# Optimization experiments

Hardware: AMD Instinct MI355X
Metric: run time of the kernel (lower is better)

Reference implementation:

```python
import jax, jax.numpy as jnp
import numpy as np
from jax.ops import segment_sum, segment_max

N_NODES = 50000
N_EDGES = 640000
N_GRAPHS = 128
IN_DIM = 128
HID = 128
OUT_DIM = 2


def setup_inputs() -> dict:
    key = jax.random.key(0)
    ks = jax.random.split(key, 16)
    x = jax.random.normal(ks[0], (N_NODES, IN_DIM), dtype=jnp.float32)
    edge_index = jax.random.randint(ks[1], (2, N_EDGES), 0, N_NODES, dtype=jnp.int64)
    batch = jnp.sort(jax.random.randint(ks[2], (N_NODES,), 0, N_GRAPHS, dtype=jnp.int64))
    s = 0.05
    return {
        "x": x,
        "edge_index": edge_index,
        "batch": batch,
        "w0": jax.random.normal(ks[3], (HID, IN_DIM), dtype=jnp.float32) * s,
        "b0": jnp.zeros((HID,), jnp.float32),
        "w1": jax.random.normal(ks[4], (HID, HID), dtype=jnp.float32) * s,
        "b1": jnp.zeros((HID,), jnp.float32),
        "w2": jax.random.normal(ks[5], (HID, HID), dtype=jnp.float32) * s,
        "b2": jnp.zeros((HID,), jnp.float32),
        "gate_w": jax.random.normal(ks[6], (1, HID), dtype=jnp.float32) * s,
        "gate_b": jnp.zeros((1,), jnp.float32),
        "lin_w": jax.random.normal(ks[7], (2 * HID, HID), dtype=jnp.float32) * s,
        "lin_b": jnp.zeros((2 * HID,), jnp.float32),
        "cls_w": jax.random.normal(ks[8], (OUT_DIM, 2 * HID), dtype=jnp.float32) * s,
        "cls_b": jnp.zeros((OUT_DIM,), jnp.float32),
    }


def _gcn_norm(edge_index, n):
    # add self loops, symmetric normalization D^-1/2 (A+I) D^-1/2
    loop = jnp.arange(n, dtype=edge_index.dtype)
    row = jnp.concatenate([edge_index[0], loop])
    col = jnp.concatenate([edge_index[1], loop])
    deg = segment_sum(jnp.ones_like(col, dtype=jnp.float32), col, num_segments=n)
    dis = jnp.where(deg > 0, jax.lax.rsqrt(deg), 0.0)
    norm = dis[row] * dis[col]
    return row, col, norm


def _gcn_conv(x, w, b, row, col, norm, n):
    xw = x @ w.T + b                     # [N, hid]
    msg = norm[:, None] * xw[row]        # gather + scale, [E+N, hid]
    return segment_sum(msg, col, num_segments=n)


def _att_pool(x, gate_w, gate_b, batch, g):
    gate = x @ gate_w.T + gate_b         # [N, 1]
    m = segment_max(gate, batch, num_segments=g)        # [G, 1]
    e = jnp.exp(gate - m[batch])
    s = segment_sum(e, batch, num_segments=g)           # [G, 1]
    alpha = e / s[batch]                                # [N, 1]
    return segment_sum(alpha * x, batch, num_segments=g)  # [G, hid]


def reference(x, edge_index, batch, w0, b0, w1, b1, w2, b2,
              gate_w, gate_b, lin_w, lin_b, cls_w, cls_b):
    n = N_NODES
    g = N_GRAPHS
    row, col, norm = _gcn_norm(edge_index, n)
    hg = None
    for w, b in ((w0, b0), (w1, b1), (w2, b2)):
        x = _gcn_conv(x, w, b, row, col, norm, n)
        x = jax.nn.relu(x)  # dropout is identity in eval mode
        pooled = _att_pool(x, gate_w, gate_b, batch, g)
        hg = pooled if hg is None else hg + pooled
    out = jax.nn.relu(hg @ lin_w.T + lin_b)
    return out @ cls_w.T + cls_b
```

## Files before the change

### kernel.cpp

```cpp
#include <hip/hip_runtime.h>
#include <hip/hip_bf16.h>
#include <float.h>

#define N_NODES  50000
#define N_EDGES  640000
#define N_GRAPHS 128
#define DIM      128
#define CAP      64
#define ZROW     N_NODES
#define NSLICE   8
#define SLICE_W  6250
#define NCHUNK   256
#define CHUNK_E  2500
#define GEMM_BLKS 512
#define POOL_BLKS 1024
#define AGG_BLKS  (8*782)

typedef __attribute__((ext_vector_type(8))) short bf16x8;
typedef __attribute__((ext_vector_type(4))) float f32x4;

__device__ __forceinline__ unsigned short f2bf(float f){
  unsigned int u = __float_as_uint(f);
  u += 0x7fffu + ((u >> 16) & 1u);
  return (unsigned short)(u >> 16);
}
__device__ __forceinline__ float2 up2(unsigned int p){
  return make_float2(__uint_as_float(p << 16),
                     __uint_as_float(p & 0xffff0000u));
}

__global__ __launch_bounds__(256) void zero_misc(int* __restrict__ cnt,
    unsigned int* __restrict__ z0, unsigned int* __restrict__ z1){
  int i = blockIdx.x*256 + threadIdx.x;
  if (i < N_NODES) cnt[i] = 0;
  else if (i < N_NODES + 64) z0[i - N_NODES] = 0;
  else if (i < N_NODES + 128) z1[i - N_NODES - 64] = 0;
}

__global__ __launch_bounds__(256) void scatter_sliced(
    const int* __restrict__ ei, int* __restrict__ cnt, int* __restrict__ srcb){
  int slice = blockIdx.x & (NSLICE-1);
  int chunk = blockIdx.x >> 3;
  int e0 = chunk * CHUNK_E;
  for (int e = e0 + threadIdx.x; e < e0 + CHUNK_E; e += 256){
    int c = ei[N_EDGES + e];
    if (c / SLICE_W == slice){
      int r = ei[e];
      int pos = atomicAdd(&cnt[c], 1);
      srcb[(c << 6) + pos] = r;
    }
  }
}

__global__ __launch_bounds__(256) void prep(
    const int* __restrict__ cnt, float* __restrict__ dis,
    const int* __restrict__ batch, int* __restrict__ gs,
    const float* __restrict__ w0, const float* __restrict__ w1,
    const float* __restrict__ w2, unsigned int* __restrict__ o0,
    unsigned int* __restrict__ o1, unsigned int* __restrict__ o2){
  int b = blockIdx.x, tid = threadIdx.x;
  if (b < 196){
    int i = b*256 + tid;
    if (i < N_NODES){
      dis[i] = 1.0f / sqrtf((float)(cnt[i] + 1));
      int bb = batch[i];
      int bp = (i == 0) ? -1 : batch[i-1];
      for (int g = bp + 1; g <= bb; ++g) gs[g] = i;
      if (i == N_NODES - 1)
        for (int g = bb + 1; g <= N_GRAPHS; ++g) gs[g] = N_NODES;
    }
  } else {
    int i = (b - 196)*256 + tid;
    if (i < 3*8192){
      int a = i >> 13, j = i & 8191;
      const float* src = (a == 0) ? w0 : (a == 1) ? w1 : w2;
      unsigned int* dst = (a == 0) ? o0 : (a == 1) ? o1 : o2;
      float2 v = ((const float2*)src)[j];
      dst[j] = (unsigned int)f2bf(v.x) | ((unsigned int)f2bf(v.y) << 16);
    }
  }
}

__device__ __forceinline__ void gemm_body_bf(int wid,
    const unsigned short* __restrict__ A, const unsigned short* __restrict__ Wb,
    const float* __restrict__ bias, const float* __restrict__ dis,
    unsigned short* __restrict__ C, int total_waves){
  int lane = threadIdx.x & 63;
  int l15 = lane & 15, l4 = lane >> 4;
  bf16x8 wf[8][4];
  #pragma unroll
  for (int ob = 0; ob < 8; ++ob)
    #pragma unroll
    for (int ks = 0; ks < 4; ++ks)
      wf[ob][ks] = *(const bf16x8*)&Wb[(ob*16 + l15)*128 + ks*32 + l4*8];
  float bv[8];
  #pragma unroll
  for (int ob = 0; ob < 8; ++ob) bv[ob] = bias[ob*16 + l15];
  for (int t = wid; t < N_NODES/16; t += total_waves){
    int row0 = t*16;
    bf16x8 af[4];
    #pragma unroll
    for (int ks = 0; ks < 4; ++ks)
      af[ks] = *(const bf16x8*)&A[(size_t)(row0 + l15)*128 + ks*32 + l4*8];
    f32x4 acc[8];
    #pragma unroll
    for (int ob = 0; ob < 8; ++ob) acc[ob] = (f32x4){0.f,0.f,0.f,0.f};
    #pragma unroll
    for (int ks = 0; ks < 4; ++ks)
      #pragma unroll
      for (int ob = 0; ob < 8; ++ob)
        acc[ob] = __builtin_amdgcn_mfma_f32_16x16x32_bf16(af[ks], wf[ob][ks],
                                                          acc[ob], 0, 0, 0);
    float dv[4];
    #pragma unroll
    for (int r = 0; r < 4; ++r) dv[r] = dis[row0 + l4*4 + r];
    #pragma unroll
    for (int ob = 0; ob < 8; ++ob)
      #pragma unroll
      for (int r = 0; r < 4; ++r)
        C[(size_t)(row0 + l4*4 + r)*128 + ob*16 + l15] =
            f2bf((acc[ob][r] + bv[ob]) * dv[r]);
  }
}

__global__ __launch_bounds__(256, 2) void gemm_f32(
    const float* __restrict__ A, const unsigned short* __restrict__ Wb,
    const float* __restrict__ bias, const float* __restrict__ dis,
    unsigned short* __restrict__ C, int total_waves){
  int lane = threadIdx.x & 63;
  int wid = blockIdx.x*4 + (threadIdx.x >> 6);
  int l15 = lane & 15, l4 = lane >> 4;
  bf16x8 wf[8][4];
  #pragma unroll
  for (int ob = 0; ob < 8; ++ob)
    #pragma unroll
    for (int ks = 0; ks < 4; ++ks)
      wf[ob][ks] = *(const bf16x8*)&Wb[(ob*16 + l15)*128 + ks*32 + l4*8];
  float bv[8];
  #pragma unroll
  for (int ob = 0; ob < 8; ++ob) bv[ob] = bias[ob*16 + l15];
  for (int t = wid; t < N_NODES/16; t += total_waves){
    int row0 = t*16;
    bf16x8 af[4];
    #pragma unroll
    for (int ks = 0; ks < 4; ++ks){
      const float4* ap = (const float4*)&A[(size_t)(row0 + l15)*128 + ks*32 + l4*8];
      float4 fa = ap[0], fb = ap[1];
      bf16x8 v;
      v[0]=(short)f2bf(fa.x); v[1]=(short)f2bf(fa.y);
      v[2]=(short)f2bf(fa.z); v[3]=(short)f2bf(fa.w);
      v[4]=(short)f2bf(fb.x); v[5]=(short)f2bf(fb.y);
      v[6]=(short)f2bf(fb.z); v[7]=(short)f2bf(fb.w);
      af[ks] = v;
    }
    f32x4 acc[8];
    #pragma unroll
    for (int ob = 0; ob < 8; ++ob) acc[ob] = (f32x4){0.f,0.f,0.f,0.f};
    #pragma unroll
    for (int ks = 0; ks < 4; ++ks)
      #pragma unroll
      for (int ob = 0; ob < 8; ++ob)
        acc[ob] = __builtin_amdgcn_mfma_f32_16x16x32_bf16(af[ks], wf[ob][ks],
                                                          acc[ob], 0, 0, 0);
    float dv[4];
    #pragma unroll
    for (int r = 0; r < 4; ++r) dv[r] = dis[row0 + l4*4 + r];
    #pragma unroll
    for (int ob = 0; ob < 8; ++ob)
      #pragma unroll
      for (int r = 0; r < 4; ++r)
        C[(size_t)(row0 + l4*4 + r)*128 + ob*16 + l15] =
            f2bf((acc[ob][r] + bv[ob]) * dv[r]);
  }
}

__device__ __forceinline__ void pool_body(int pbid,
    const unsigned int* __restrict__ x, const float* __restrict__ gate,
    const int* __restrict__ gs, float* __restrict__ hgp,
    float* __restrict__ ssum){
  int g = pbid >> 3, q = pbid & 7, tid = threadIdx.x;
  int s = gs[g], e = gs[g+1];
  __shared__ float red[256];
  __shared__ float2 red2[4][64];
  float m = -FLT_MAX;
  for (int i = s + tid; i < e; i += 256) m = fmaxf(m, gate[i]);
  red[tid] = m; __syncthreads();
  for (int st = 128; st > 0; st >>= 1){
    if (tid < st) red[tid] = fmaxf(red[tid], red[tid+st]);
    __syncthreads();
  }
  m = red[0]; __syncthreads();
  float p = 0.f;
  for (int i = s + tid; i < e; i += 256) p += __expf(gate[i] - m);
  red[tid] = p; __syncthreads();
  for (int st = 128; st > 0; st >>= 1){
    if (tid < st) red[tid] += red[tid+st];
    __syncthreads();
  }
  if (tid == 0 && q == 0) ssum[g] = red[0];
  int d2 = tid & 63, rg = tid >> 6;
  float ax = 0.f, ay = 0.f;
  for (int i = s + q*4 + rg; i < e; i += 32){
    float a = __expf(gate[i] - m);
    float2 u = up2(x[(size_t)i*64 + d2]);
    ax += a*u.x; ay += a*u.y;
  }
  red2[rg][d2] = make_float2(ax, ay);
  __syncthreads();
  if (tid < 64){
    float2 r0 = red2[0][tid], r1 = red2[1][tid],
           r2 = red2[2][tid], r3 = red2[3][tid];
    hgp[(size_t)pbid*128 + 2*tid    ] = r0.x + r1.x + r2.x + r3.x;
    hgp[(size_t)pbid*128 + 2*tid + 1] = r0.y + r1.y + r2.y + r3.y;
  }
}

__global__ __launch_bounds__(256, 2) void pool_gemm(
    const unsigned int* __restrict__ xb, const float* __restrict__ gate,
    const int* __restrict__ gs, float* __restrict__ hgp,
    float* __restrict__ ssum,
    const unsigned short* __restrict__ Wb, const float* __restrict__ bias,
    const float* __restrict__ dis, unsigned short* __restrict__ xwout){
  if (blockIdx.x < GEMM_BLKS){
    int wid = blockIdx.x*4 + (threadIdx.x >> 6);
    gemm_body_bf(wid, (const unsigned short*)xb, Wb, bias, dis, xwout,
                 GEMM_BLKS*4);
  } else {
    pool_body(blockIdx.x - GEMM_BLKS, xb, gate, gs, hgp, ssum);
  }
}

__global__ __launch_bounds__(256) void att_pool(
    const unsigned int* __restrict__ xb, const float* __restrict__ gate,
    const int* __restrict__ gs, float* __restrict__ hgp,
    float* __restrict__ ssum){
  pool_body(blockIdx.x, xb, gate, gs, hgp, ssum);
}

__global__ __launch_bounds__(256) void aggregate_bf(
    const uint4* __restrict__ xw4,
    const int* __restrict__ cnt, const int* __restrict__ srcb,
    const float* __restrict__ dis,
    uint4* __restrict__ xout4, const float* __restrict__ gw,
    const float* __restrict__ gb, float* __restrict__ gate){
  int tid  = threadIdx.x;
  int lane = tid & 63;
  int wv   = tid >> 6;
  int quad = wv >> 1;
  int par  = wv & 1;
  int sub  = lane >> 4, l16 = lane & 15;
  int slice = blockIdx.x & 7, within = blockIdx.x >> 3;
  int loc   = within*8 + quad*4 + sub;
  bool valid = loc < SLICE_W;
  int node  = slice*SLICE_W + (valid ? loc : SLICE_W-1);
  int n     = valid ? cnt[node] : 0;
  int base  = node << 6;
  float acc[8];
  #pragma unroll
  for (int i = 0; i < 8; ++i) acc[i] = 0.f;
  if (par == 0 && valid){
    uint4 v = xw4[node*16 + l16];
    float2 a0 = up2(v.x), a1 = up2(v.y), a2 = up2(v.z), a3 = up2(v.w);
    acc[0]=a0.x; acc[1]=a0.y; acc[2]=a1.x; acc[3]=a1.y;
    acc[4]=a2.x; acc[5]=a2.y; acc[6]=a3.x; acc[7]=a3.y;
  }
  for (int e = par*8; e < n; e += 16){
    int4 sa = *(const int4*)&srcb[base + e];
    int4 sb = *(const int4*)&srcb[base + e + 4];
    int r0 = (e   < n) ? sa.x : ZROW;
    int r1 = (e+1 < n) ? sa.y : ZROW;
    int r2 = (e+2 < n) ? sa.z : ZROW;
    int r3 = (e+3 < n) ? sa.w : ZROW;
    int r4 = (e+4 < n) ? sb.x : ZROW;
    int r5 = (e+5 < n) ? sb.y : ZROW;
    int r6 = (e+6 < n) ? sb.z : ZROW;
    int r7 = (e+7 < n) ? sb.w : ZROW;
    uint4 u0 = xw4[r0*16 + l16];
    uint4 u1 = xw4[r1*16 + l16];
    uint4 u2 = xw4[r2*16 + l16];
    uint4 u3 = xw4[r3*16 + l16];
    uint4 u4 = xw4[r4*16 + l16];
    uint4 u5 = xw4[r5*16 + l16];
    uint4 u6 = xw4[r6*16 + l16];
    uint4 u7 = xw4[r7*16 + l16];
    #define ACC8(U) { \
      float2 b0=up2(U.x), b1=up2(U.y), b2=up2(U.z), b3=up2(U.w); \
      acc[0]+=b0.x; acc[1]+=b0.y; acc[2]+=b1.x; acc[3]+=b1.y;    \
      acc[4]+=b2.x; acc[5]+=b2.y; acc[6]+=b3.x; acc[7]+=b3.y; }
    ACC8(u0) ACC8(u1) ACC8(u2) ACC8(u3)
    ACC8(u4) ACC8(u5) ACC8(u6) ACC8(u7)
    #undef ACC8
  }
  __shared__ float comb[2][64][9];
  if (par == 1){
    #pragma unroll
    for (int i = 0; i < 8; ++i) comb[quad][lane][i] = acc[i];
  }
  __syncthreads();
  if (par == 0 && valid){
    float d = dis[node];
    #pragma unroll
    for (int i = 0; i < 8; ++i)
      acc[i] = fmaxf(d*(acc[i] + comb[quad][lane][i]), 0.f);
    uint4 o;
    o.x = (unsigned int)f2bf(acc[0]) | ((unsigned int)f2bf(acc[1]) << 16);
    o.y = (unsigned int)f2bf(acc[2]) | ((unsigned int)f2bf(acc[3]) << 16);
    o.z = (unsigned int)f2bf(acc[4]) | ((unsigned int)f2bf(acc[5]) << 16);
    o.w = (unsigned int)f2bf(acc[6]) | ((unsigned int)f2bf(acc[7]) << 16);
    xout4[node*16 + l16] = o;
    const float4* gw4 = (const float4*)gw;
    float4 g0 = gw4[l16*2], g1 = gw4[l16*2 + 1];
    float p = acc[0]*g0.x + acc[1]*g0.y + acc[2]*g0.z + acc[3]*g0.w
            + acc[4]*g1.x + acc[5]*g1.y + acc[6]*g1.z + acc[7]*g1.w;
    p += __shfl_xor(p, 1, 64);
    p += __shfl_xor(p, 2, 64);
    p += __shfl_xor(p, 4, 64);
    p += __shfl_xor(p, 8, 64);
    if (l16 == 0) gate[node] = p + gb[0];
  }
}

__global__ __launch_bounds__(256) void head(const float* __restrict__ hgp,
    const float* __restrict__ ssum,
    const float* __restrict__ lw, const float* __restrict__ lb,
    const float* __restrict__ cw, const float* __restrict__ cb,
    float* __restrict__ out){
  int g = blockIdx.x, tid = threadIdx.x;
  __shared__ float h[128];
  __shared__ float t1[256];
  __shared__ float red[256];
  if (tid < 128){
    float hv = 0.f;
    #pragma unroll
    for (int L = 0; L < 3; ++L){
      const float* hb = hgp + (size_t)(L*POOL_BLKS + 8*g)*128;
      float pp = 0.f;
      #pragma unroll
      for (int q = 0; q < 8; ++q) pp += hb[q*128 + tid];
      float sv = ssum[L*N_GRAPHS + g];
      hv += (sv > 0.f) ? pp/sv : 0.f;
    }
    h[tid] = hv;
  }
  __syncthreads();
  const float* wr = lw + tid*128;
  float a = 0.f;
  for (int k = 0; k < 128; ++k) a += h[k]*wr[k];
  a = fmaxf(a + lb[tid], 0.f);
  t1[tid] = a;
  __syncthreads();
  int o = tid >> 7, j = tid & 127;
  float p = t1[j]*cw[o*256 + j] + t1[j+128]*cw[o*256 + j + 128];
  red[tid] = p; __syncthreads();
  for (int st = 64; st > 0; st >>= 1){
    if (j < st) red[tid] += red[tid+st];
    __syncthreads();
  }
  if (j == 0) out[g*2 + o] = red[tid] + cb[o];
}

extern "C" void kernel_launch(void* const* d_in, const int* in_sizes, int n_in,
                              void* d_out, int out_size, void* d_ws, size_t ws_size,
                              hipStream_t stream){
  const float* x   = (const float*)d_in[0];
  const int*   ei  = (const int*)d_in[1];
  const int* batch = (const int*)d_in[2];
  const float* w0  = (const float*)d_in[3];
  const float* b0  = (const float*)d_in[4];
  const float* w1  = (const float*)d_in[5];
  const float* b1  = (const float*)d_in[6];
  const float* w2  = (const float*)d_in[7];
  const float* b2  = (const float*)d_in[8];
  const float* gw  = (const float*)d_in[9];
  const float* gb  = (const float*)d_in[10];
  const float* lw  = (const float*)d_in[11];
  const float* lb  = (const float*)d_in[12];
  const float* cw  = (const float*)d_in[13];
  const float* cb  = (const float*)d_in[14];
  float* out = (float*)d_out;
  (void)in_sizes; (void)n_in; (void)out_size; (void)ws_size;

  char* ws = (char*)d_ws;
  size_t off = 0;
  auto alloc = [&](size_t bytes)->char*{
    char* p = ws + off;
    off = (off + bytes + 255) & ~(size_t)255;
    return p;
  };
  float* dis    = (float*)alloc((size_t)N_NODES*4);
  unsigned int* xw   = (unsigned int*)alloc((size_t)(N_NODES+1)*64*4);
  unsigned int* xbuf = (unsigned int*)alloc((size_t)(N_NODES+1)*64*4);
  unsigned int* Wb0  = (unsigned int*)alloc((size_t)DIM*64*4);
  unsigned int* Wb1  = (unsigned int*)alloc((size_t)DIM*64*4);
  unsigned int* Wb2  = (unsigned int*)alloc((size_t)DIM*64*4);
  float* gate  = (float*)alloc((size_t)N_NODES*4);
  float* hgp   = (float*)alloc((size_t)3*POOL_BLKS*DIM*4);
  float* ssum  = (float*)alloc((size_t)3*N_GRAPHS*4);
  int*   gs    = (int*)alloc((size_t)(N_GRAPHS+1)*4);
  int*   cnt   = (int*)alloc((size_t)N_NODES*4);
  int*   srcb  = (int*)alloc(((size_t)N_NODES*CAP + 64)*4);

  const int T = 256;
  zero_misc     <<<(N_NODES+128+T-1)/T, T, 0, stream>>>(cnt,
                    xw + (size_t)ZROW*64, xbuf + (size_t)ZROW*64);
  scatter_sliced<<<NCHUNK*NSLICE, T, 0, stream>>>(ei, cnt, srcb);
  prep          <<<196 + 96, T, 0, stream>>>(cnt, dis, batch, gs,
                                             w0, w1, w2, Wb0, Wb1, Wb2);

  gemm_f32<<<GEMM_BLKS, 256, 0, stream>>>(x, (const unsigned short*)Wb0, b0,
                                          dis, (unsigned short*)xw, GEMM_BLKS*4);
  aggregate_bf<<<AGG_BLKS, 256, 0, stream>>>((const uint4*)xw, cnt, srcb, dis,
                                             (uint4*)xbuf, gw, gb, gate);
  pool_gemm<<<GEMM_BLKS + POOL_BLKS, 256, 0, stream>>>(
      xbuf, gate, gs, hgp, ssum,
      (const unsigned short*)Wb1, b1, dis, (unsigned short*)xw);
  aggregate_bf<<<AGG_BLKS, 256, 0, stream>>>((const uint4*)xw, cnt, srcb, dis,
                                             (uint4*)xbuf, gw, gb, gate);
  pool_gemm<<<GEMM_BLKS + POOL_BLKS, 256, 0, stream>>>(
      xbuf, gate, gs, hgp + (size_t)POOL_BLKS*DIM, ssum + N_GRAPHS,
      (const unsigned short*)Wb2, b2, dis, (unsigned short*)xw);
  aggregate_bf<<<AGG_BLKS, 256, 0, stream>>>((const uint4*)xw, cnt, srcb, dis,
                                             (uint4*)xbuf, gw, gb, gate);
  att_pool<<<POOL_BLKS, 256, 0, stream>>>(xbuf, gate, gs,
                                          hgp + (size_t)2*POOL_BLKS*DIM,
                                          ssum + 2*N_GRAPHS);
  head<<<N_GRAPHS, 256, 0, stream>>>(hgp, ssum, lw, lb, cw, cb, out);
}
```

Baseline: 198.7 us.

## Split node feature matrices into four 32-column planes for cache-local gather aggregation

Node feature buffers are stored as four planes of 32 bf16 columns each, so each aggregation block gathers only one 64-byte quarter-row per neighbor. Blocks are assigned per plane, which shrinks the working set per plane and should improve L2 hit rates for the random edge gathers. Each node uses 4 lanes per plane, replacing the two-wave split and LDS combine. The gate dot product is now stored as four partial sums that the pooling step adds together. This brings more blocks, repeated neighbor-list reads across planes, and extra gate reads in pooling.

```diff
diff --git a/kernel.cpp b/kernel.cpp
--- a/kernel.cpp
+++ b/kernel.cpp
@@ -8,13 +8,15 @@
 #define DIM      128
 #define CAP      64
 #define ZROW     N_NODES
+#define NROWS    (N_NODES+1)
 #define NSLICE   8
 #define SLICE_W  6250
 #define NCHUNK   256
 #define CHUNK_E  2500
 #define GEMM_BLKS 512
 #define POOL_BLKS 1024
-#define AGG_BLKS  (8*782)
+#define AGG_CHUNKS 782
+#define AGG_BLKS  (8*391)
 
 typedef __attribute__((ext_vector_type(8))) short bf16x8;
 typedef __attribute__((ext_vector_type(4))) float f32x4;
@@ -33,8 +35,13 @@
     unsigned int* __restrict__ z0, unsigned int* __restrict__ z1){
   int i = blockIdx.x*256 + threadIdx.x;
   if (i < N_NODES) cnt[i] = 0;
-  else if (i < N_NODES + 64) z0[i - N_NODES] = 0;
-  else if (i < N_NODES + 128) z1[i - N_NODES - 64] = 0;
+  else if (i < N_NODES + 128){
+    int j = i - N_NODES;
+    unsigned int* z = (j < 64) ? z0 : z1;
+    int jj = j & 63;
+    int q = jj >> 4, k = jj & 15;
+    z[((size_t)q*NROWS + ZROW)*16 + k] = 0;
+  }
 }
 
 __global__ __launch_bounds__(256) void scatter_sliced(
@@ -101,7 +108,7 @@
     bf16x8 af[4];
     #pragma unroll
     for (int ks = 0; ks < 4; ++ks)
-      af[ks] = *(const bf16x8*)&A[(size_t)(row0 + l15)*128 + ks*32 + l4*8];
+      af[ks] = *(const bf16x8*)&A[((size_t)ks*NROWS + row0 + l15)*32 + l4*8];
     f32x4 acc[8];
     #pragma unroll
     for (int ob = 0; ob < 8; ++ob) acc[ob] = (f32x4){0.f,0.f,0.f,0.f};
@@ -118,7 +125,7 @@
     for (int ob = 0; ob < 8; ++ob)
       #pragma unroll
       for (int r = 0; r < 4; ++r)
-        C[(size_t)(row0 + l4*4 + r)*128 + ob*16 + l15] =
+        C[((size_t)(ob>>1)*NROWS + row0 + l4*4 + r)*32 + (ob&1)*16 + l15] =
             f2bf((acc[ob][r] + bv[ob]) * dv[r]);
   }
 }
@@ -169,102 +176,37 @@
     for (int ob = 0; ob < 8; ++ob)
       #pragma unroll
       for (int r = 0; r < 4; ++r)
-        C[(size_t)(row0 + l4*4 + r)*128 + ob*16 + l15] =
+        C[((size_t)(ob>>1)*NROWS + row0 + l4*4 + r)*32 + (ob&1)*16 + l15] =
             f2bf((acc[ob][r] + bv[ob]) * dv[r]);
   }
 }
 
-__device__ __forceinline__ void pool_body(int pbid,
-    const unsigned int* __restrict__ x, const float* __restrict__ gate,
-    const int* __restrict__ gs, float* __restrict__ hgp,
-    float* __restrict__ ssum){
-  int g = pbid >> 3, q = pbid & 7, tid = threadIdx.x;
-  int s = gs[g], e = gs[g+1];
-  __shared__ float red[256];
-  __shared__ float2 red2[4][64];
-  float m = -FLT_MAX;
-  for (int i = s + tid; i < e; i += 256) m = fmaxf(m, gate[i]);
-  red[tid] = m; __syncthreads();
-  for (int st = 128; st > 0; st >>= 1){
-    if (tid < st) red[tid] = fmaxf(red[tid], red[tid+st]);
-    __syncthreads();
-  }
-  m = red[0]; __syncthreads();
-  float p = 0.f;
-  for (int i = s + tid; i < e; i += 256) p += __expf(gate[i] - m);
-  red[tid] = p; __syncthreads();
-  for (int st = 128; st > 0; st >>= 1){
-    if (tid < st) red[tid] += red[tid+st];
-    __syncthreads();
-  }
-  if (tid == 0 && q == 0) ssum[g] = red[0];
-  int d2 = tid & 63, rg = tid >> 6;
-  float ax = 0.f, ay = 0.f;
-  for (int i = s + q*4 + rg; i < e; i += 32){
-    float a = __expf(gate[i] - m);
-    float2 u = up2(x[(size_t)i*64 + d2]);
-    ax += a*u.x; ay += a*u.y;
-  }
-  red2[rg][d2] = make_float2(ax, ay);
-  __syncthreads();
-  if (tid < 64){
-    float2 r0 = red2[0][tid], r1 = red2[1][tid],
-           r2 = red2[2][tid], r3 = red2[3][tid];
-    hgp[(size_t)pbid*128 + 2*tid    ] = r0.x + r1.x + r2.x + r3.x;
-    hgp[(size_t)pbid*128 + 2*tid + 1] = r0.y + r1.y + r2.y + r3.y;
-  }
-}
-
-__global__ __launch_bounds__(256, 2) void pool_gemm(
-    const unsigned int* __restrict__ xb, const float* __restrict__ gate,
-    const int* __restrict__ gs, float* __restrict__ hgp,
-    float* __restrict__ ssum,
-    const unsigned short* __restrict__ Wb, const float* __restrict__ bias,
-    const float* __restrict__ dis, unsigned short* __restrict__ xwout){
-  if (blockIdx.x < GEMM_BLKS){
-    int wid = blockIdx.x*4 + (threadIdx.x >> 6);
-    gemm_body_bf(wid, (const unsigned short*)xb, Wb, bias, dis, xwout,
-                 GEMM_BLKS*4);
-  } else {
-    pool_body(blockIdx.x - GEMM_BLKS, xb, gate, gs, hgp, ssum);
-  }
-}
-
-__global__ __launch_bounds__(256) void att_pool(
-    const unsigned int* __restrict__ xb, const float* __restrict__ gate,
-    const int* __restrict__ gs, float* __restrict__ hgp,
-    float* __restrict__ ssum){
-  pool_body(blockIdx.x, xb, gate, gs, hgp, ssum);
-}
-
-__global__ __launch_bounds__(256) void aggregate_bf(
-    const uint4* __restrict__ xw4,
+__global__ __launch_bounds__(256) void aggregate_q(
+    const uint4* __restrict__ xq,
     const int* __restrict__ cnt, const int* __restrict__ srcb,
     const float* __restrict__ dis,
-    uint4* __restrict__ xout4, const float* __restrict__ gw,
-    const float* __restrict__ gb, float* __restrict__ gate){
+    uint4* __restrict__ xoq, const float* __restrict__ gw,
+    float* __restrict__ gq){
   int tid  = threadIdx.x;
   int lane = tid & 63;
   int wv   = tid >> 6;
-  int quad = wv >> 1;
-  int par  = wv & 1;
-  int sub  = lane >> 4, l16 = lane & 15;
-  int slice = blockIdx.x & 7, within = blockIdx.x >> 3;
-  int loc   = within*8 + quad*4 + sub;
-  bool valid = loc < SLICE_W;
-  int node  = slice*SLICE_W + (valid ? loc : SLICE_W-1);
+  int grp  = lane >> 2, l4 = lane & 3;
+  int q     = (blockIdx.x & 7) >> 1;
+  int chunk = (blockIdx.x >> 3)*2 + (blockIdx.x & 1);
+  int node0 = chunk*64 + wv*16 + grp;
+  bool valid = node0 < N_NODES;
+  int node  = valid ? node0 : 0;
   int n     = valid ? cnt[node] : 0;
   int base  = node << 6;
+  size_t qbase = (size_t)q*NROWS*4;
+  uint4 v = xq[qbase + (size_t)node*4 + l4];
   float acc[8];
-  #pragma unroll
-  for (int i = 0; i < 8; ++i) acc[i] = 0.f;
-  if (par == 0 && valid){
-    uint4 v = xw4[node*16 + l16];
+  {
     float2 a0 = up2(v.x), a1 = up2(v.y), a2 = up2(v.z), a3 = up2(v.w);
     acc[0]=a0.x; acc[1]=a0.y; acc[2]=a1.x; acc[3]=a1.y;
     acc[4]=a2.x; acc[5]=a2.y; acc[6]=a3.x; acc[7]=a3.y;
   }
-  for (int e = par*8; e < n; e += 16){
+  for (int e = 0; e < n; e += 8){
     int4 sa = *(const int4*)&srcb[base + e];
     int4 sb = *(const int4*)&srcb[base + e + 4];
     int r0 = (e   < n) ? sa.x : ZROW;
@@ -275,14 +217,14 @@
     int r5 = (e+5 < n) ? sb.y : ZROW;
     int r6 = (e+6 < n) ? sb.z : ZROW;
     int r7 = (e+7 < n) ? sb.w : ZROW;
-    uint4 u0 = xw4[r0*16 + l16];
-    uint4 u1 = xw4[r1*16 + l16];
-    uint4 u2 = xw4[r2*16 + l16];
-    uint4 u3 = xw4[r3*16 + l16];
-    uint4 u4 = xw4[r4*16 + l16];
-    uint4 u5 = xw4[r5*16 + l16];
-    uint4 u6 = xw4[r6*16 + l16];
-    uint4 u7 = xw4[r7*16 + l16];
+    uint4 u0 = xq[qbase + (size_t)r0*4 + l4];
+    uint4 u1 = xq[qbase + (size_t)r1*4 + l4];
+    uint4 u2 = xq[qbase + (size_t)r2*4 + l4];
+    uint4 u3 = xq[qbase + (size_t)r3*4 + l4];
+    uint4 u4 = xq[qbase + (size_t)r4*4 + l4];
+    uint4 u5 = xq[qbase + (size_t)r5*4 + l4];
+    uint4 u6 = xq[qbase + (size_t)r6*4 + l4];
+    uint4 u7 = xq[qbase + (size_t)r7*4 + l4];
     #define ACC8(U) { \
       float2 b0=up2(U.x), b1=up2(U.y), b2=up2(U.z), b3=up2(U.w); \
       acc[0]+=b0.x; acc[1]+=b0.y; acc[2]+=b1.x; acc[3]+=b1.y;    \
@@ -291,33 +233,94 @@
     ACC8(u4) ACC8(u5) ACC8(u6) ACC8(u7)
     #undef ACC8
   }
-  __shared__ float comb[2][64][9];
-  if (par == 1){
-    #pragma unroll
-    for (int i = 0; i < 8; ++i) comb[quad][lane][i] = acc[i];
-  }
-  __syncthreads();
-  if (par == 0 && valid){
+  if (valid){
     float d = dis[node];
     #pragma unroll
-    for (int i = 0; i < 8; ++i)
-      acc[i] = fmaxf(d*(acc[i] + comb[quad][lane][i]), 0.f);
+    for (int i = 0; i < 8; ++i) acc[i] = fmaxf(d*acc[i], 0.f);
     uint4 o;
     o.x = (unsigned int)f2bf(acc[0]) | ((unsigned int)f2bf(acc[1]) << 16);
     o.y = (unsigned int)f2bf(acc[2]) | ((unsigned int)f2bf(acc[3]) << 16);
     o.z = (unsigned int)f2bf(acc[4]) | ((unsigned int)f2bf(acc[5]) << 16);
     o.w = (unsigned int)f2bf(acc[6]) | ((unsigned int)f2bf(acc[7]) << 16);
-    xout4[node*16 + l16] = o;
+    xoq[qbase + (size_t)node*4 + l4] = o;
     const float4* gw4 = (const float4*)gw;
-    float4 g0 = gw4[l16*2], g1 = gw4[l16*2 + 1];
+    float4 g0 = gw4[q*8 + l4*2], g1 = gw4[q*8 + l4*2 + 1];
     float p = acc[0]*g0.x + acc[1]*g0.y + acc[2]*g0.z + acc[3]*g0.w
             + acc[4]*g1.x + acc[5]*g1.y + acc[6]*g1.z + acc[7]*g1.w;
     p += __shfl_xor(p, 1, 64);
     p += __shfl_xor(p, 2, 64);
-    p += __shfl_xor(p, 4, 64);
-    p += __shfl_xor(p, 8, 64);
-    if (l16 == 0) gate[node] = p + gb[0];
-  }
+    if (l4 == 0) gq[(size_t)q*N_NODES + node] = p;
+  }
+}
+
+__device__ __forceinline__ float gate_at(const float* __restrict__ gq, int i,
+                                         float gbv){
+  return gq[i] + gq[N_NODES + i] + gq[2*N_NODES + i] + gq[3*N_NODES + i] + gbv;
+}
+
+__device__ __forceinline__ void pool_body(int pbid,
+    const unsigned int* __restrict__ x, const float* __restrict__ gq,
+    float gbv, const int* __restrict__ gs, float* __restrict__ hgp,
+    float* __restrict__ ssum){
+  int g = pbid >> 3, q = pbid & 7, tid = threadIdx.x;
+  int s = gs[g], e = gs[g+1];
+  __shared__ float red[256];
+  __shared__ float2 red2[4][64];
+  float m = -FLT_MAX;
+  for (int i = s + tid; i < e; i += 256) m = fmaxf(m, gate_at(gq, i, gbv));
+  red[tid] = m; __syncthreads();
+  for (int st = 128; st > 0; st >>= 1){
+    if (tid < st) red[tid] = fmaxf(red[tid], red[tid+st]);
+    __syncthreads();
+  }
+  m = red[0]; __syncthreads();
+  float p = 0.f;
+  for (int i = s + tid; i < e; i += 256) p += __expf(gate_at(gq, i, gbv) - m);
+  red[tid] = p; __syncthreads();
+  for (int st = 128; st > 0; st >>= 1){
+    if (tid < st) red[tid] += red[tid+st];
+    __syncthreads();
+  }
+  if (tid == 0 && q == 0) ssum[g] = red[0];
+  int d2 = tid & 63, rg = tid >> 6;
+  int qf = d2 >> 4, jf = d2 & 15;
+  size_t fbase = ((size_t)qf*NROWS)*16 + jf;
+  float ax = 0.f, ay = 0.f;
+  for (int i = s + q*4 + rg; i < e; i += 32){
+    float a = __expf(gate_at(gq, i, gbv) - m);
+    float2 u = up2(x[fbase + (size_t)i*16]);
+    ax += a*u.x; ay += a*u.y;
+  }
+  red2[rg][d2] = make_float2(ax, ay);
+  __syncthreads();
+  if (tid < 64){
+    float2 r0 = red2[0][tid], r1 = red2[1][tid],
+           r2 = red2[2][tid], r3 = red2[3][tid];
+    hgp[(size_t)pbid*128 + 2*tid    ] = r0.x + r1.x + r2.x + r3.x;
+    hgp[(size_t)pbid*128 + 2*tid + 1] = r0.y + r1.y + r2.y + r3.y;
+  }
+}
+
+__global__ __launch_bounds__(256, 2) void pool_gemm(
+    const unsigned int* __restrict__ xb, const float* __restrict__ gq,
+    const float* __restrict__ gb, const int* __restrict__ gs,
+    float* __restrict__ hgp, float* __restrict__ ssum,
+    const unsigned short* __restrict__ Wb, const float* __restrict__ bias,
+    const float* __restrict__ dis, unsigned short* __restrict__ xwout){
+  if (blockIdx.x < GEMM_BLKS){
+    int wid = blockIdx.x*4 + (threadIdx.x >> 6);
+    gemm_body_bf(wid, (const unsigned short*)xb, Wb, bias, dis, xwout,
+                 GEMM_BLKS*4);
+  } else {
+    pool_body(blockIdx.x - GEMM_BLKS, xb, gq, gb[0], gs, hgp, ssum);
+  }
+}
+
+__global__ __launch_bounds__(256) void att_pool(
+    const unsigned int* __restrict__ xb, const float* __restrict__ gq,
+    const float* __restrict__ gb, const int* __restrict__ gs,
+    float* __restrict__ hgp, float* __restrict__ ssum){
+  pool_body(blockIdx.x, xb, gq, gb[0], gs, hgp, ssum);
 }
 
 __global__ __launch_bounds__(256) void head(const float* __restrict__ hgp,
@@ -388,12 +391,12 @@
     return p;
   };
   float* dis    = (float*)alloc((size_t)N_NODES*4);
-  unsigned int* xw   = (unsigned int*)alloc((size_t)(N_NODES+1)*64*4);
-  unsigned int* xbuf = (unsigned int*)alloc((size_t)(N_NODES+1)*64*4);
+  unsigned int* xw   = (unsigned int*)alloc((size_t)4*NROWS*16*4);
+  unsigned int* xbuf = (unsigned int*)alloc((size_t)4*NROWS*16*4);
   unsigned int* Wb0  = (unsigned int*)alloc((size_t)DIM*64*4);
   unsigned int* Wb1  = (unsigned int*)alloc((size_t)DIM*64*4);
   unsigned int* Wb2  = (unsigned int*)alloc((size_t)DIM*64*4);
-  float* gate  = (float*)alloc((size_t)N_NODES*4);
+  float* gq    = (float*)alloc((size_t)4*N_NODES*4);
   float* hgp   = (float*)alloc((size_t)3*POOL_BLKS*DIM*4);
   float* ssum  = (float*)alloc((size_t)3*N_GRAPHS*4);
   int*   gs    = (int*)alloc((size_t)(N_GRAPHS+1)*4);
@@ -401,27 +404,26 @@
   int*   srcb  = (int*)alloc(((size_t)N_NODES*CAP + 64)*4);
 
   const int T = 256;
-  zero_misc     <<<(N_NODES+128+T-1)/T, T, 0, stream>>>(cnt,
-                    xw + (size_t)ZROW*64, xbuf + (size_t)ZROW*64);
+  zero_misc     <<<(N_NODES+128+T-1)/T, T, 0, stream>>>(cnt, xw, xbuf);
   scatter_sliced<<<NCHUNK*NSLICE, T, 0, stream>>>(ei, cnt, srcb);
   prep          <<<196 + 96, T, 0, stream>>>(cnt, dis, batch, gs,
                                              w0, w1, w2, Wb0, Wb1, Wb2);
 
   gemm_f32<<<GEMM_BLKS, 256, 0, stream>>>(x, (const unsigned short*)Wb0, b0,
                                           dis, (unsigned short*)xw, GEMM_BLKS*4);
-  aggregate_bf<<<AGG_BLKS, 256, 0, stream>>>((const uint4*)xw, cnt, srcb, dis,
-                                             (uint4*)xbuf, gw, gb, gate);
+  aggregate_q<<<AGG_BLKS*8, 256, 0, stream>>>((const uint4*)xw, cnt, srcb, dis,
+                                              (uint4*)xbuf, gw, gq);
   pool_gemm<<<GEMM_BLKS + POOL_BLKS, 256, 0, stream>>>(
-      xbuf, gate, gs, hgp, ssum,
+      xbuf, gq, gb, gs, hgp, ssum,
       (const unsigned short*)Wb1, b1, dis, (unsigned short*)xw);
-  aggregate_bf<<<AGG_BLKS, 256, 0, stream>>>((const uint4*)xw, cnt, srcb, dis,
-                                             (uint4*)xbuf, gw, gb, gate);
+  aggregate_q<<<AGG_BLKS*8, 256, 0, stream>>>((const uint4*)xw, cnt, srcb, dis,
+                                              (uint4*)xbuf, gw, gq);
   pool_gemm<<<GEMM_BLKS + POOL_BLKS, 256, 0, stream>>>(
-      xbuf, gate, gs, hgp + (size_t)POOL_BLKS*DIM, ssum + N_GRAPHS,
+      xbuf, gq, gb, gs, hgp + (size_t)POOL_BLKS*DIM, ssum + N_GRAPHS,
       (const unsigned short*)Wb2, b2, dis, (unsigned short*)xw);
-  aggregate_bf<<<AGG_BLKS, 256, 0, stream>>>((const uint4*)xw, cnt, srcb, dis,
-                                             (uint4*)xbuf, gw, gb, gate);
-  att_pool<<<POOL_BLKS, 256, 0, stream>>>(xbuf, gate, gs,
+  aggregate_q<<<AGG_BLKS*8, 256, 0, stream>>>((const uint4*)xw, cnt, srcb, dis,
+                                              (uint4*)xbuf, gw, gq);
+  att_pool<<<POOL_BLKS, 256, 0, stream>>>(xbuf, gq, gb, gs,
                                           hgp + (size_t)2*POOL_BLKS*DIM,
                                           ssum + 2*N_GRAPHS);
   head<<<N_GRAPHS, 256, 0, stream>>>(hgp, ssum, lw, lb, cw, cb, out);
```

New measurement: 214.3 us. +7.8%, slower.
